# Kernel tuning notes

Measured on AMD Instinct MI355X. Metric: run time of the kernel, lower is better.

## Reference

```python
import jax, jax.numpy as jnp
import numpy as np

B, S, N = 1, 128, 256
D_MSA, D_PAIR, D_HID = 256, 128, 32
EPS = 1e-3
LN_EPS = 1e-5


def _layer_norm(x, w, b):
    mu = jnp.mean(x, axis=-1, keepdims=True)
    var = jnp.mean(jnp.square(x - mu), axis=-1, keepdims=True)
    return (x - mu) * jax.lax.rsqrt(var + LN_EPS) * w + b


def setup_inputs() -> dict:
    key = jax.random.key(0)
    ks = jax.random.split(key, 8)
    sc = lambda fan_in: (1.0 / fan_in) ** 0.5
    return {
        "m": jax.random.normal(ks[0], (B, S, N, D_MSA), dtype=jnp.float32),
        "mask": jnp.ones((B, S, N), dtype=jnp.float32),
        "ln_w": jnp.ones((D_MSA,), dtype=jnp.float32),
        "ln_b": jnp.zeros((D_MSA,), dtype=jnp.float32),
        "w1": jax.random.normal(ks[1], (D_HID, D_MSA), dtype=jnp.float32) * sc(D_MSA),
        "b1": jnp.zeros((D_HID,), dtype=jnp.float32),
        "w2": jax.random.normal(ks[2], (D_HID, D_MSA), dtype=jnp.float32) * sc(D_MSA),
        "b2": jnp.zeros((D_HID,), dtype=jnp.float32),
        "w_out": jax.random.normal(ks[3], (D_PAIR, D_HID * D_HID), dtype=jnp.float32) * sc(D_HID * D_HID),
        "b_out": jnp.zeros((D_PAIR,), dtype=jnp.float32),
        "ln_out_w": jnp.ones((D_PAIR,), dtype=jnp.float32),
        "ln_out_b": jnp.zeros((D_PAIR,), dtype=jnp.float32),
        "wz": jax.random.normal(ks[4], (D_PAIR, D_PAIR), dtype=jnp.float32) * sc(D_PAIR),
        "bz": jnp.zeros((D_PAIR,), dtype=jnp.float32),
    }


def reference(m, mask, ln_w, ln_b, w1, b1, w2, b2, w_out, b_out, ln_out_w, ln_out_b, wz, bz):
    # m: [B, S, N, d_msa], mask: [B, S, N]
    x = _layer_norm(m, ln_w, ln_b)
    n_res = mask.shape[-1]
    mk = mask[..., None] * (n_res ** -0.5)          # [B, S, N, 1] (layer_norm_out branch)
    a = (jnp.einsum('bsnd,hd->bsnh', x, w1) + b1) * mk
    b_ = (jnp.einsum('bsnd,hd->bsnh', x, w2) + b2) * mk
    a = jnp.swapaxes(a, -2, -3)                      # [B, N, S, h]
    b_ = jnp.swapaxes(b_, -2, -3)                    # [B, N, S, h]
    outer = jnp.einsum('bisc,bjse->bijce', a, b_)    # [B, N, N, h, h]
    outer = outer.reshape(outer.shape[:-2] + (-1,))  # [B, N, N, h*h]
    z = jnp.einsum('bijk,pk->bijp', outer, w_out) + b_out  # [B, N, N, d_pair]
    norm = jnp.einsum('bsi,bsj->bij', mk[..., 0], mk[..., 0])[..., None]
    z = z / (EPS + norm)
    z = jax.nn.gelu(z, approximate=False)
    z = _layer_norm(z, ln_out_w, ln_out_b)
    z = jnp.einsum('bijp,qp->bijq', z, wz) + bz
    return z
```

## Files before the change

### kernel.cpp

```cpp
#include <hip/hip_runtime.h>
#include <hip/hip_bf16.h>
#include <math.h>

#define EPSC 1e-3f

typedef __attribute__((ext_vector_type(8))) short short8;
typedef __attribute__((ext_vector_type(4))) float float4v;

static __device__ __forceinline__ unsigned short f2bf(float f) {
    union { float f; unsigned u; } x; x.f = f;
    unsigned r = x.u + 0x7FFFu + ((x.u >> 16) & 1u);
    return (unsigned short)(r >> 16);
}

static __device__ __forceinline__ unsigned pk_bf16(float lo, float hi) {
    union { __hip_bfloat162 h; unsigned u; } cv;
    cv.h = __float22bfloat162_rn(make_float2(lo, hi));
    return cv.u;
}

static __device__ __forceinline__ float4v mfma16(short8 a, short8 b, float4v c) {
    return __builtin_amdgcn_mfma_f32_16x16x32_bf16(a, b, c, 0, 0, 0);
}

#define OFF_NORM 0ull
#define OFF_AT   262144ull
#define OFF_BT   2359296ull
#define OFF_WOF  4456448ull
#define OFF_WZF  4718592ull
#define OFF_W12  4751360ull

__global__ __launch_bounds__(256) void k_norm(const float* __restrict__ mask,
                                              float* __restrict__ normw) {
    int i = blockIdx.x, j = threadIdx.x;
    float acc = 0.f;
#pragma unroll 8
    for (int s = 0; s < 128; ++s)
        acc += mask[s * 256 + i] * mask[s * 256 + j];
    normw[i * 256 + j] = acc * (1.0f / 256.0f);
}

__global__ __launch_bounds__(256) void k_cvt(const float* __restrict__ w_out,
                                             const float* __restrict__ wz,
                                             const float* __restrict__ w1,
                                             const float* __restrict__ w2,
                                             unsigned short* __restrict__ wobF,
                                             unsigned short* __restrict__ wzF,
                                             unsigned short* __restrict__ w12F) {
    int idx = blockIdx.x * 256 + threadIdx.x;
    if (idx < 131072) {
        int j = idx & 7, lane = (idx >> 3) & 63, kk = (idx >> 9) & 31, w = idx >> 14;
        int p = w * 16 + (lane & 15);
        int k = kk * 32 + (lane >> 4) * 8 + j;
        wobF[idx] = f2bf(w_out[p * 1024 + k]);
    } else if (idx < 147456) {
        int q = idx - 131072;
        int j = q & 7, lane = (q >> 3) & 63, kk = (q >> 9) & 3, w = q >> 11;
        int p = w * 16 + (lane & 15);
        int k = kk * 32 + (lane >> 4) * 8 + j;
        wzF[q] = f2bf(wz[p * 128 + k]);
    } else if (idx < 163840) {
        int q = idx - 147456;
        int j = q & 7, lane = (q >> 3) & 63, ht = (q >> 9) & 3, kk = q >> 11;
        int h = ht * 16 + (lane & 15);
        int d = kk * 32 + (lane >> 4) * 8 + j;
        w12F[q] = f2bf(h < 32 ? w1[h * 256 + d] : w2[(h - 32) * 256 + d]);
    }
}

__global__ __launch_bounds__(256) void k1_lnproj(
    const float* __restrict__ m, const float* __restrict__ mask,
    const float* __restrict__ ln_w, const float* __restrict__ ln_b,
    const float* __restrict__ b1, const float* __restrict__ b2,
    const unsigned short* __restrict__ w12F,
    unsigned short* __restrict__ aT, unsigned short* __restrict__ bT)
{
    __shared__ unsigned short xs[64 * 264];
    __shared__ unsigned short tr[64 * 76];
    __shared__ float mkl[64];
    __shared__ float b12[64];
    int t = threadIdx.x;
    int w = t >> 6, lane = t & 63;
    int g = lane >> 4, l15 = lane & 15;
    int n0 = (blockIdx.x & 31) * 8, s0 = (blockIdx.x >> 5) * 8;

    if (t < 64) {
        b12[t] = (t < 32) ? b1[t] : b2[t - 32];
        mkl[t] = mask[(s0 + (t >> 3)) * 256 + n0 + (t & 7)] * 0.0625f;
    }

    float4 lwv = *(const float4*)(ln_w + lane * 4);
    float4 lbv = *(const float4*)(ln_b + lane * 4);

    for (int i = 0; i < 16; ++i) {
        int r = w * 16 + i;
        size_t gr = (size_t)(s0 + (r >> 3)) * 256 + n0 + (r & 7);
        float4 v = *(const float4*)(m + gr * 256 + lane * 4);
        float sum = v.x + v.y + v.z + v.w;
        float sq = v.x * v.x + v.y * v.y + v.z * v.z + v.w * v.w;
#pragma unroll
        for (int off = 32; off > 0; off >>= 1) {
            sum += __shfl_xor(sum, off, 64);
            sq  += __shfl_xor(sq, off, 64);
        }
        float mu = sum * (1.f / 256.f);
        float rstd = rsqrtf(sq * (1.f / 256.f) - mu * mu + 1e-5f);
        uint2 u;
        u.x = pk_bf16((v.x - mu) * rstd * lwv.x + lbv.x, (v.y - mu) * rstd * lwv.y + lbv.y);
        u.y = pk_bf16((v.z - mu) * rstd * lwv.z + lbv.z, (v.w - mu) * rstd * lwv.w + lbv.w);
        *(uint2*)(xs + r * 264 + lane * 4) = u;
    }
    __syncthreads();

    float4v zf = {0.f, 0.f, 0.f, 0.f};
    float4v acc[4]; acc[0] = zf; acc[1] = zf; acc[2] = zf; acc[3] = zf;
#pragma unroll
    for (int kk = 0; kk < 8; ++kk) {
        short8 af = *(const short8*)(xs + (w * 16 + l15) * 264 + kk * 32 + g * 8);
#pragma unroll
        for (int ht = 0; ht < 4; ++ht) {
            short8 bfr = *(const short8*)(w12F + ((size_t)(kk * 4 + ht) * 64 + lane) * 8);
            acc[ht] = mfma16(af, bfr, acc[ht]);
        }
    }
#pragma unroll
    for (int ht = 0; ht < 4; ++ht) {
        int h = ht * 16 + l15;
        float bias = b12[h];
        int rbase = w * 16 + g * 4;
        uint2 u;
        u.x = pk_bf16((acc[ht][0] + bias) * mkl[rbase + 0], (acc[ht][1] + bias) * mkl[rbase + 1]);
        u.y = pk_bf16((acc[ht][2] + bias) * mkl[rbase + 2], (acc[ht][3] + bias) * mkl[rbase + 3]);
        *(uint2*)(tr + h * 76 + rbase) = u;
    }
    __syncthreads();

#pragma unroll
    for (int it = 0; it < 2; ++it) {
        int q = t + it * 256;
        int h = q >> 3, n_l = q & 7;
        unsigned short vv[8];
#pragma unroll
        for (int s_l = 0; s_l < 8; ++s_l)
            vv[s_l] = tr[h * 76 + s_l * 8 + n_l];
        uint4 u;
        u.x = (unsigned)vv[0] | ((unsigned)vv[1] << 16);
        u.y = (unsigned)vv[2] | ((unsigned)vv[3] << 16);
        u.z = (unsigned)vv[4] | ((unsigned)vv[5] << 16);
        u.w = (unsigned)vv[6] | ((unsigned)vv[7] << 16);
        unsigned short* dst = ((h < 32) ? aT : bT) + ((size_t)(n0 + n_l) * 32 + (h & 31)) * 128 + s0;
        *(uint4*)dst = u;
    }
}

__global__ __launch_bounds__(512, 2) void k2_fused(
    const unsigned short* __restrict__ aT, const unsigned short* __restrict__ bT,
    const unsigned short* __restrict__ wobF, const unsigned short* __restrict__ wzF,
    const float* __restrict__ b_out, const float* __restrict__ normw,
    const float* __restrict__ ln_ow, const float* __restrict__ ln_ob,
    const float* __restrict__ bz, float* __restrict__ out)
{
    __shared__ char smem[131072];
    unsigned short* As = (unsigned short*)smem;
    unsigned short* Bs = (unsigned short*)(smem + 36864);
    unsigned* oL = (unsigned*)smem;
    float* zL = (float*)smem;
    unsigned short* lnL = (unsigned short*)(smem + 36864);

    int t = threadIdx.x;
    int w = t >> 6, lane = t & 63;
    int g = lane >> 4, l15 = lane & 15;
    int bj = blockIdx.x, bi = blockIdx.y;
    int wn = w & 1, wm = w >> 1;

    const unsigned short* Ag = aT + (size_t)bi * 256 * 128;
    const unsigned short* Bg = bT + (size_t)bj * 256 * 128;

    float4v zf = {0.f, 0.f, 0.f, 0.f};
    float4v acc[4][8];
#pragma unroll
    for (int fm = 0; fm < 4; ++fm)
#pragma unroll
        for (int fn = 0; fn < 8; ++fn) acc[fm][fn] = zf;

    for (int p = 0; p < 2; ++p) {
        if (p) __syncthreads();
#pragma unroll
        for (int it = 0; it < 4; ++it) {
            int q = t + it * 512;
            int row = q >> 3, c8 = q & 7;
            *(uint4*)(As + row * 72 + c8 * 8) = *(const uint4*)(Ag + row * 128 + p * 64 + c8 * 8);
            *(uint4*)(Bs + row * 72 + c8 * 8) = *(const uint4*)(Bg + row * 128 + p * 64 + c8 * 8);
        }
        __syncthreads();
#pragma unroll
        for (int kk2 = 0; kk2 < 2; ++kk2) {
            short8 af[4], bf[8];
#pragma unroll
            for (int fm = 0; fm < 4; ++fm)
                af[fm] = *(const short8*)(As + (wm * 64 + fm * 16 + l15) * 72 + kk2 * 32 + g * 8);
#pragma unroll
            for (int fn = 0; fn < 8; ++fn)
                bf[fn] = *(const short8*)(Bs + (wn * 128 + fn * 16 + l15) * 72 + kk2 * 32 + g * 8);
#pragma unroll
            for (int fm = 0; fm < 4; ++fm)
#pragma unroll
                for (int fn = 0; fn < 8; ++fn)
                    acc[fm][fn] = mfma16(bf[fn], af[fm], acc[fm][fn]);
        }
    }
    __syncthreads();

#pragma unroll
    for (int fm = 0; fm < 4; ++fm) {
#pragma unroll
        for (int fn = 0; fn < 8; ++fn) {
            int pair = (wm * 2 + (fm >> 1)) * 8 + wn * 4 + (fn >> 1);
            int c_in = (fm & 1) * 16 + l15;
            int o = (fn & 1) * 8 + 2 * g;
            int dw = pair * 512 + ((c_in * 16 + o) ^ ((pair & 7) << 2));
            float4v a4 = acc[fm][fn];
            uint2 u;
            u.x = pk_bf16(a4[0], a4[1]);
            u.y = pk_bf16(a4[2], a4[3]);
            *(uint2*)(oL + dw) = u;
        }
    }
    __syncthreads();

    float4v acc2[4]; acc2[0] = zf; acc2[1] = zf; acc2[2] = zf; acc2[3] = zf;
    const unsigned short* wbase = wobF + (size_t)w * 16384;
#pragma unroll 8
    for (int kk = 0; kk < 32; ++kk) {
        short8 bfw = *(const short8*)(wbase + (kk * 64 + lane) * 8);
#pragma unroll
        for (int fr = 0; fr < 4; ++fr) {
            int dw = (fr * 16 + l15) * 512 + ((kk * 16 + g * 4) ^ ((l15 & 7) << 2));
            short8 af2 = *(const short8*)(oL + dw);
            acc2[fr] = mfma16(af2, bfw, acc2[fr]);
        }
    }
    __syncthreads();
#pragma unroll
    for (int fr = 0; fr < 4; ++fr)
#pragma unroll
        for (int r = 0; r < 4; ++r)
            zL[(fr * 16 + g * 4 + r) * 132 + w * 16 + l15] = acc2[fr][r];
    __syncthreads();

    {
        const float4 loA = *(const float4*)(ln_ow + l15 * 8);
        const float4 loB = *(const float4*)(ln_ow + l15 * 8 + 4);
        const float4 lbA = *(const float4*)(ln_ob + l15 * 8);
        const float4 lbB = *(const float4*)(ln_ob + l15 * 8 + 4);
        const float4 boA = *(const float4*)(b_out + l15 * 8);
        const float4 boB = *(const float4*)(b_out + l15 * 8 + 4);
        float lw8[8] = {loA.x, loA.y, loA.z, loA.w, loB.x, loB.y, loB.z, loB.w};
        float lb8[8] = {lbA.x, lbA.y, lbA.z, lbA.w, lbB.x, lbB.y, lbB.z, lbB.w};
        float bo8[8] = {boA.x, boA.y, boA.z, boA.w, boB.x, boB.y, boB.z, boB.w};
#pragma unroll
        for (int it = 0; it < 2; ++it) {
            int pair = w * 8 + it * 4 + g;
            int iG = bi * 8 + (pair >> 3), jG = bj * 8 + (pair & 7);
            float inv = 1.0f / (EPSC + normw[iG * 256 + jG]);
            float4v z0 = *(const float4v*)(zL + pair * 132 + l15 * 8);
            float4v z1 = *(const float4v*)(zL + pair * 132 + l15 * 8 + 4);
            float vals[8];
            float sum = 0.f, sq = 0.f;
#pragma unroll
            for (int e2 = 0; e2 < 8; ++e2) {
                float v = ((e2 < 4) ? z0[e2] : z1[e2 - 4]) + bo8[e2];
                v *= inv;
                v = 0.5f * v * (1.0f + erff(v * 0.70710678118654752f));
                vals[e2] = v; sum += v; sq += v * v;
            }
#pragma unroll
            for (int mm = 1; mm <= 8; mm <<= 1) {
                sum += __shfl_xor(sum, mm);
                sq  += __shfl_xor(sq, mm);
            }
            float mu = sum * (1.0f / 128.0f);
            float rstd = rsqrtf(sq * (1.0f / 128.0f) - mu * mu + 1e-5f);
            uint4 upk;
            upk.x = pk_bf16((vals[0] - mu) * rstd * lw8[0] + lb8[0],
                            (vals[1] - mu) * rstd * lw8[1] + lb8[1]);
            upk.y = pk_bf16((vals[2] - mu) * rstd * lw8[2] + lb8[2],
                            (vals[3] - mu) * rstd * lw8[3] + lb8[3]);
            upk.z = pk_bf16((vals[4] - mu) * rstd * lw8[4] + lb8[4],
                            (vals[5] - mu) * rstd * lw8[5] + lb8[5]);
            upk.w = pk_bf16((vals[6] - mu) * rstd * lw8[6] + lb8[6],
                            (vals[7] - mu) * rstd * lw8[7] + lb8[7]);
            *(uint4*)(lnL + pair * 136 + l15 * 8) = upk;
        }
    }
    __syncthreads();

    float4v acc3[4]; acc3[0] = zf; acc3[1] = zf; acc3[2] = zf; acc3[3] = zf;
#pragma unroll
    for (int kk = 0; kk < 4; ++kk) {
        short8 bfw = *(const short8*)(wzF + ((size_t)(w * 4 + kk) * 64 + lane) * 8);
#pragma unroll
        for (int fr = 0; fr < 4; ++fr) {
            short8 af3 = *(const short8*)(lnL + (fr * 16 + l15) * 136 + kk * 32 + g * 8);
            acc3[fr] = mfma16(af3, bfw, acc3[fr]);
        }
    }
    {
        float bzq = bz[w * 16 + l15];
#pragma unroll
        for (int fr = 0; fr < 4; ++fr) {
#pragma unroll
            for (int r = 0; r < 4; ++r) {
                int pair = fr * 16 + g * 4 + r;
                int row = (bi * 8 + (pair >> 3)) * 256 + bj * 8 + (pair & 7);
                out[(size_t)row * 128 + w * 16 + l15] = acc3[fr][r] + bzq;
            }
        }
    }
}

extern "C" void kernel_launch(void* const* d_in, const int* in_sizes, int n_in,
                              void* d_out, int out_size, void* d_ws, size_t ws_size,
                              hipStream_t stream) {
    const float* m      = (const float*)d_in[0];
    const float* mask   = (const float*)d_in[1];
    const float* ln_w   = (const float*)d_in[2];
    const float* ln_b   = (const float*)d_in[3];
    const float* w1     = (const float*)d_in[4];
    const float* b1     = (const float*)d_in[5];
    const float* w2     = (const float*)d_in[6];
    const float* b2     = (const float*)d_in[7];
    const float* w_out  = (const float*)d_in[8];
    const float* b_out  = (const float*)d_in[9];
    const float* ln_ow  = (const float*)d_in[10];
    const float* ln_ob  = (const float*)d_in[11];
    const float* wz     = (const float*)d_in[12];
    const float* bz     = (const float*)d_in[13];
    float* out = (float*)d_out;
    char*  ws  = (char*)d_ws;

    float* normw          = (float*)(ws + OFF_NORM);
    unsigned short* aTb   = (unsigned short*)(ws + OFF_AT);
    unsigned short* bTb   = (unsigned short*)(ws + OFF_BT);
    unsigned short* wobF  = (unsigned short*)(ws + OFF_WOF);
    unsigned short* wzF   = (unsigned short*)(ws + OFF_WZF);
    unsigned short* w12F  = (unsigned short*)(ws + OFF_W12);

    k_norm<<<dim3(256), dim3(256), 0, stream>>>(mask, normw);
    k_cvt<<<dim3(640), dim3(256), 0, stream>>>(w_out, wz, w1, w2, wobF, wzF, w12F);
    k1_lnproj<<<dim3(512), dim3(256), 0, stream>>>(m, mask, ln_w, ln_b, b1, b2, w12F, aTb, bTb);
    k2_fused<<<dim3(32, 32), dim3(512), 0, stream>>>(aTb, bTb, wobF, wzF, b_out, normw,
                                                     ln_ow, ln_ob, bz, out);
}
```

Before: 184.1 us.

## Merge prep kernels, load full K tile once, use 32x32 MFMA for w_out GEMM

Folds the norm and weight-conversion kernels into the LN/projection kernel as extra blocks, leaving a tiny separate w1/w2 conversion kernel. The pair kernel now loads the whole 128-deep A/B tiles into swizzled LDS at once instead of two staged halves. The w_out contraction switches to 32x32x16 MFMA with a matching weight layout and adjusted swizzle. This reduces launch overhead and syncs, but the w12F write in k_pre duplicates the conversion (and races with reads of w12F_in in the same launch, though the values are identical). A static __global__ function declared inside a local struct is unusual HIP and may not compile.

```diff
diff --git a/kernel.cpp b/kernel.cpp
--- a/kernel.cpp
+++ b/kernel.cpp
@@ -4,23 +4,25 @@
 
 #define EPSC 1e-3f
 
-typedef __attribute__((ext_vector_type(8))) short short8;
-typedef __attribute__((ext_vector_type(4))) float float4v;
+typedef __attribute__((ext_vector_type(8)))  short  short8;
+typedef __attribute__((ext_vector_type(4)))  float  float4v;
+typedef __attribute__((ext_vector_type(16))) float  float16v;
 
 static __device__ __forceinline__ unsigned short f2bf(float f) {
     union { float f; unsigned u; } x; x.f = f;
     unsigned r = x.u + 0x7FFFu + ((x.u >> 16) & 1u);
     return (unsigned short)(r >> 16);
 }
-
 static __device__ __forceinline__ unsigned pk_bf16(float lo, float hi) {
     union { __hip_bfloat162 h; unsigned u; } cv;
     cv.h = __float22bfloat162_rn(make_float2(lo, hi));
     return cv.u;
 }
-
 static __device__ __forceinline__ float4v mfma16(short8 a, short8 b, float4v c) {
     return __builtin_amdgcn_mfma_f32_16x16x32_bf16(a, b, c, 0, 0, 0);
+}
+static __device__ __forceinline__ float16v mfma32(short8 a, short8 b, float16v c) {
+    return __builtin_amdgcn_mfma_f32_32x32x16_bf16(a, b, c, 0, 0, 0);
 }
 
 #define OFF_NORM 0ull
@@ -30,59 +32,60 @@
 #define OFF_WZF  4718592ull
 #define OFF_W12  4751360ull
 
-__global__ __launch_bounds__(256) void k_norm(const float* __restrict__ mask,
-                                              float* __restrict__ normw) {
-    int i = blockIdx.x, j = threadIdx.x;
-    float acc = 0.f;
-#pragma unroll 8
-    for (int s = 0; s < 128; ++s)
-        acc += mask[s * 256 + i] * mask[s * 256 + j];
-    normw[i * 256 + j] = acc * (1.0f / 256.0f);
-}
-
-__global__ __launch_bounds__(256) void k_cvt(const float* __restrict__ w_out,
-                                             const float* __restrict__ wz,
-                                             const float* __restrict__ w1,
-                                             const float* __restrict__ w2,
-                                             unsigned short* __restrict__ wobF,
-                                             unsigned short* __restrict__ wzF,
-                                             unsigned short* __restrict__ w12F) {
-    int idx = blockIdx.x * 256 + threadIdx.x;
-    if (idx < 131072) {
-        int j = idx & 7, lane = (idx >> 3) & 63, kk = (idx >> 9) & 31, w = idx >> 14;
-        int p = w * 16 + (lane & 15);
-        int k = kk * 32 + (lane >> 4) * 8 + j;
-        wobF[idx] = f2bf(w_out[p * 1024 + k]);
-    } else if (idx < 147456) {
-        int q = idx - 131072;
-        int j = q & 7, lane = (q >> 3) & 63, kk = (q >> 9) & 3, w = q >> 11;
-        int p = w * 16 + (lane & 15);
-        int k = kk * 32 + (lane >> 4) * 8 + j;
-        wzF[q] = f2bf(wz[p * 128 + k]);
-    } else if (idx < 163840) {
-        int q = idx - 147456;
-        int j = q & 7, lane = (q >> 3) & 63, ht = (q >> 9) & 3, kk = q >> 11;
-        int h = ht * 16 + (lane & 15);
-        int d = kk * 32 + (lane >> 4) * 8 + j;
-        w12F[q] = f2bf(h < 32 ? w1[h * 256 + d] : w2[(h - 32) * 256 + d]);
-    }
-}
-
-__global__ __launch_bounds__(256) void k1_lnproj(
+__global__ __launch_bounds__(256) void k_pre(
     const float* __restrict__ m, const float* __restrict__ mask,
     const float* __restrict__ ln_w, const float* __restrict__ ln_b,
-    const float* __restrict__ b1, const float* __restrict__ b2,
-    const unsigned short* __restrict__ w12F,
-    unsigned short* __restrict__ aT, unsigned short* __restrict__ bT)
+    const float* __restrict__ w1, const float* __restrict__ b1,
+    const float* __restrict__ w2, const float* __restrict__ b2,
+    const float* __restrict__ w_out, const float* __restrict__ wz,
+    unsigned short* __restrict__ aT, unsigned short* __restrict__ bT,
+    unsigned short* __restrict__ wobF, unsigned short* __restrict__ wzF,
+    const unsigned short* __restrict__ w12F_in,
+    unsigned short* __restrict__ w12F,
+    float* __restrict__ normw)
 {
     __shared__ unsigned short xs[64 * 264];
     __shared__ unsigned short tr[64 * 76];
     __shared__ float mkl[64];
     __shared__ float b12[64];
     int t = threadIdx.x;
+    int b = blockIdx.x;
+
+    if (b >= 1152) {
+        int i = b - 1152, j = t;
+        float acc = 0.f;
+#pragma unroll 8
+        for (int s = 0; s < 128; ++s)
+            acc += mask[s * 256 + i] * mask[s * 256 + j];
+        normw[i * 256 + j] = acc * (1.0f / 256.0f);
+        return;
+    }
+    if (b >= 512) {
+        int idx = (b - 512) * 256 + t;
+        if (idx < 131072) {
+            int j = idx & 7, lane = (idx >> 3) & 63, k16 = (idx >> 9) & 63, pw = idx >> 15;
+            int p = pw * 32 + (lane & 31);
+            int k = k16 * 16 + (lane >> 5) * 8 + j;
+            wobF[idx] = f2bf(w_out[p * 1024 + k]);
+        } else if (idx < 147456) {
+            int q = idx - 131072;
+            int j = q & 7, lane = (q >> 3) & 63, kk = (q >> 9) & 3, w = q >> 11;
+            int p = w * 16 + (lane & 15);
+            int k = kk * 32 + (lane >> 4) * 8 + j;
+            wzF[q] = f2bf(wz[p * 128 + k]);
+        } else if (idx < 163840) {
+            int q = idx - 147456;
+            int j = q & 7, lane = (q >> 3) & 63, ht = (q >> 9) & 3, kk = q >> 11;
+            int h = ht * 16 + (lane & 15);
+            int d = kk * 32 + (lane >> 4) * 8 + j;
+            w12F[q] = f2bf(h < 32 ? w1[h * 256 + d] : w2[(h - 32) * 256 + d]);
+        }
+        return;
+    }
+
     int w = t >> 6, lane = t & 63;
     int g = lane >> 4, l15 = lane & 15;
-    int n0 = (blockIdx.x & 31) * 8, s0 = (blockIdx.x >> 5) * 8;
+    int n0 = (b & 31) * 8, s0 = (b >> 5) * 8;
 
     if (t < 64) {
         b12[t] = (t < 32) ? b1[t] : b2[t - 32];
@@ -92,6 +95,7 @@
     float4 lwv = *(const float4*)(ln_w + lane * 4);
     float4 lbv = *(const float4*)(ln_b + lane * 4);
 
+#pragma unroll 4
     for (int i = 0; i < 16; ++i) {
         int r = w * 16 + i;
         size_t gr = (size_t)(s0 + (r >> 3)) * 256 + n0 + (r & 7);
@@ -112,14 +116,14 @@
     }
     __syncthreads();
 
-    float4v zf = {0.f, 0.f, 0.f, 0.f};
-    float4v acc[4]; acc[0] = zf; acc[1] = zf; acc[2] = zf; acc[3] = zf;
+    float4v zf4 = {0.f, 0.f, 0.f, 0.f};
+    float4v acc[4]; acc[0] = zf4; acc[1] = zf4; acc[2] = zf4; acc[3] = zf4;
 #pragma unroll
     for (int kk = 0; kk < 8; ++kk) {
         short8 af = *(const short8*)(xs + (w * 16 + l15) * 264 + kk * 32 + g * 8);
 #pragma unroll
         for (int ht = 0; ht < 4; ++ht) {
-            short8 bfr = *(const short8*)(w12F + ((size_t)(kk * 4 + ht) * 64 + lane) * 8);
+            short8 bfr = *(const short8*)(w12F_in + ((size_t)(kk * 4 + ht) * 64 + lane) * 8);
             acc[ht] = mfma16(af, bfr, acc[ht]);
         }
     }
@@ -161,8 +165,7 @@
     const float* __restrict__ bz, float* __restrict__ out)
 {
     __shared__ char smem[131072];
-    unsigned short* As = (unsigned short*)smem;
-    unsigned short* Bs = (unsigned short*)(smem + 36864);
+    unsigned* s32 = (unsigned*)smem;
     unsigned* oL = (unsigned*)smem;
     float* zL = (float*)smem;
     unsigned short* lnL = (unsigned short*)(smem + 36864);
@@ -173,35 +176,43 @@
     int bj = blockIdx.x, bi = blockIdx.y;
     int wn = w & 1, wm = w >> 1;
 
-    const unsigned short* Ag = aT + (size_t)bi * 256 * 128;
-    const unsigned short* Bg = bT + (size_t)bj * 256 * 128;
-
-    float4v zf = {0.f, 0.f, 0.f, 0.f};
+    {
+        const uint4* Agv = (const uint4*)(aT + (size_t)bi * 256 * 128);
+        const uint4* Bgv = (const uint4*)(bT + (size_t)bj * 256 * 128);
+#pragma unroll
+        for (int it = 0; it < 8; ++it) {
+            int q = t + it * 512;
+            int row = q >> 4, col4 = (q & 15) * 4;
+            int dcol = col4 ^ ((row & 7) << 2);
+            *(uint4*)(s32 + row * 64 + dcol) = Agv[q];
+            *(uint4*)(s32 + 16384 + row * 64 + dcol) = Bgv[q];
+        }
+    }
+    __syncthreads();
+
+    float4v zf4 = {0.f, 0.f, 0.f, 0.f};
     float4v acc[4][8];
 #pragma unroll
     for (int fm = 0; fm < 4; ++fm)
 #pragma unroll
-        for (int fn = 0; fn < 8; ++fn) acc[fm][fn] = zf;
-
-    for (int p = 0; p < 2; ++p) {
-        if (p) __syncthreads();
-#pragma unroll
-        for (int it = 0; it < 4; ++it) {
-            int q = t + it * 512;
-            int row = q >> 3, c8 = q & 7;
-            *(uint4*)(As + row * 72 + c8 * 8) = *(const uint4*)(Ag + row * 128 + p * 64 + c8 * 8);
-            *(uint4*)(Bs + row * 72 + c8 * 8) = *(const uint4*)(Bg + row * 128 + p * 64 + c8 * 8);
-        }
-        __syncthreads();
-#pragma unroll
-        for (int kk2 = 0; kk2 < 2; ++kk2) {
+        for (int fn = 0; fn < 8; ++fn) acc[fm][fn] = zf4;
+
+    {
+        int sw = (l15 & 7) << 2;
+#pragma unroll
+        for (int kk = 0; kk < 4; ++kk) {
+            int col = (kk * 16 + g * 4) ^ sw;
             short8 af[4], bf[8];
 #pragma unroll
-            for (int fm = 0; fm < 4; ++fm)
-                af[fm] = *(const short8*)(As + (wm * 64 + fm * 16 + l15) * 72 + kk2 * 32 + g * 8);
-#pragma unroll
-            for (int fn = 0; fn < 8; ++fn)
-                bf[fn] = *(const short8*)(Bs + (wn * 128 + fn * 16 + l15) * 72 + kk2 * 32 + g * 8);
+            for (int fm = 0; fm < 4; ++fm) {
+                int row = wm * 64 + fm * 16 + l15;
+                af[fm] = *(const short8*)((const char*)(s32 + row * 64 + col));
+            }
+#pragma unroll
+            for (int fn = 0; fn < 8; ++fn) {
+                int row = wn * 128 + fn * 16 + l15;
+                bf[fn] = *(const short8*)((const char*)(s32 + 16384 + row * 64 + col));
+            }
 #pragma unroll
             for (int fm = 0; fm < 4; ++fm)
 #pragma unroll
@@ -216,9 +227,10 @@
 #pragma unroll
         for (int fn = 0; fn < 8; ++fn) {
             int pair = (wm * 2 + (fm >> 1)) * 8 + wn * 4 + (fn >> 1);
-            int c_in = (fm & 1) * 16 + l15;
+            int c = (fm & 1) * 16 + l15;
             int o = (fn & 1) * 8 + 2 * g;
-            int dw = pair * 512 + ((c_in * 16 + o) ^ ((pair & 7) << 2));
+            int off = c * 16 + o;
+            int dw = pair * 512 + (off ^ ((((pair & 7) ^ (off >> 6)) & 7) << 2));
             float4v a4 = acc[fm][fn];
             uint2 u;
             u.x = pk_bf16(a4[0], a4[1]);
@@ -228,24 +240,29 @@
     }
     __syncthreads();
 
-    float4v acc2[4]; acc2[0] = zf; acc2[1] = zf; acc2[2] = zf; acc2[3] = zf;
-    const unsigned short* wbase = wobF + (size_t)w * 16384;
+    {
+        int pw = w & 3, ph = w >> 2;
+        int l31 = lane & 31, h2 = lane >> 5;
+        int pairR = ph * 32 + l31;
+        int prebase = pairR * 512;
+        int psw = (pairR & 7);
+        float16v acc32 = {0.f};
+        const unsigned short* wbase = wobF + (size_t)pw * 32768;
 #pragma unroll 8
-    for (int kk = 0; kk < 32; ++kk) {
-        short8 bfw = *(const short8*)(wbase + (kk * 64 + lane) * 8);
-#pragma unroll
-        for (int fr = 0; fr < 4; ++fr) {
-            int dw = (fr * 16 + l15) * 512 + ((kk * 16 + g * 4) ^ ((l15 & 7) << 2));
-            short8 af2 = *(const short8*)(oL + dw);
-            acc2[fr] = mfma16(af2, bfw, acc2[fr]);
-        }
-    }
-    __syncthreads();
-#pragma unroll
-    for (int fr = 0; fr < 4; ++fr)
-#pragma unroll
-        for (int r = 0; r < 4; ++r)
-            zL[(fr * 16 + g * 4 + r) * 132 + w * 16 + l15] = acc2[fr][r];
+        for (int k16 = 0; k16 < 64; ++k16) {
+            int off = k16 * 8 + h2 * 4;
+            int dw = prebase + (off ^ (((psw ^ (off >> 6)) & 7) << 2));
+            short8 a2 = *(const short8*)((const char*)(oL + dw));
+            short8 b2 = *(const short8*)(wbase + ((size_t)(k16 * 64 + lane)) * 8);
+            acc32 = mfma32(a2, b2, acc32);
+        }
+        __syncthreads();
+#pragma unroll
+        for (int reg = 0; reg < 16; ++reg) {
+            int prow = ph * 32 + (reg & 3) + 8 * (reg >> 2) + 4 * h2;
+            zL[prow * 132 + pw * 32 + l31] = acc32[reg];
+        }
+    }
     __syncthreads();
 
     {
@@ -295,17 +312,17 @@
     }
     __syncthreads();
 
-    float4v acc3[4]; acc3[0] = zf; acc3[1] = zf; acc3[2] = zf; acc3[3] = zf;
-#pragma unroll
-    for (int kk = 0; kk < 4; ++kk) {
-        short8 bfw = *(const short8*)(wzF + ((size_t)(w * 4 + kk) * 64 + lane) * 8);
-#pragma unroll
-        for (int fr = 0; fr < 4; ++fr) {
-            short8 af3 = *(const short8*)(lnL + (fr * 16 + l15) * 136 + kk * 32 + g * 8);
-            acc3[fr] = mfma16(af3, bfw, acc3[fr]);
-        }
-    }
-    {
+    {
+        float4v acc3[4]; acc3[0] = zf4; acc3[1] = zf4; acc3[2] = zf4; acc3[3] = zf4;
+#pragma unroll
+        for (int kk = 0; kk < 4; ++kk) {
+            short8 bfw = *(const short8*)(wzF + ((size_t)(w * 4 + kk) * 64 + lane) * 8);
+#pragma unroll
+            for (int fr = 0; fr < 4; ++fr) {
+                short8 af3 = *(const short8*)(lnL + (fr * 16 + l15) * 136 + kk * 32 + g * 8);
+                acc3[fr] = mfma16(af3, bfw, acc3[fr]);
+            }
+        }
         float bzq = bz[w * 16 + l15];
 #pragma unroll
         for (int fr = 0; fr < 4; ++fr) {
@@ -346,9 +363,23 @@
     unsigned short* wzF   = (unsigned short*)(ws + OFF_WZF);
     unsigned short* w12F  = (unsigned short*)(ws + OFF_W12);
 
-    k_norm<<<dim3(256), dim3(256), 0, stream>>>(mask, normw);
-    k_cvt<<<dim3(640), dim3(256), 0, stream>>>(w_out, wz, w1, w2, wobF, wzF, w12F);
-    k1_lnproj<<<dim3(512), dim3(256), 0, stream>>>(m, mask, ln_w, ln_b, b1, b2, w12F, aTb, bTb);
+    {
+        struct L {
+            static __global__ void __launch_bounds__(256) cvt12(
+                const float* __restrict__ w1, const float* __restrict__ w2,
+                unsigned short* __restrict__ w12F) {
+                int q = blockIdx.x * 256 + threadIdx.x;
+                int j = q & 7, lane = (q >> 3) & 63, ht = (q >> 9) & 3, kk = q >> 11;
+                int h = ht * 16 + (lane & 15);
+                int d = kk * 32 + (lane >> 4) * 8 + j;
+                w12F[q] = f2bf(h < 32 ? w1[h * 256 + d] : w2[(h - 32) * 256 + d]);
+            }
+        };
+        L::cvt12<<<dim3(64), dim3(256), 0, stream>>>(w1, w2, w12F);
+    }
+    k_pre<<<dim3(1408), dim3(256), 0, stream>>>(m, mask, ln_w, ln_b, w1, b1, w2, b2,
+                                                w_out, wz, aTb, bTb, wobF, wzF,
+                                                w12F, w12F, normw);
     k2_fused<<<dim3(32, 32), dim3(512), 0, stream>>>(aTb, bTb, wobF, wzF, b_out, normw,
                                                      ln_ow, ln_ob, bz, out);
 }
```

Measured after the change: 166.9 us. 1.1x faster.
